# Kernel tuning notes

Measured on AMD Instinct MI355X. Metric: run time of the kernel, lower is better.

The kernel has to match this reference:

```python
import jax, jax.numpy as jnp
import numpy as np

B, T, TR, DIM, H = 1, 4096, 1024, 1536, 12
DH = DIM // H          # 128
EPS = 1e-6             # RMSNorm eps
REF_SCALE = 1.0


def setup_inputs() -> dict:
    key = jax.random.key(0)
    ks = jax.random.split(key, 20)
    s = 0.02
    w = lambda k: jax.random.normal(k, (DIM, DIM), jnp.float32) * s
    b = lambda k: jax.random.normal(k, (DIM,), jnp.float32) * 0.01
    theta = jax.random.uniform(ks[2], (T, DH // 2), jnp.float32) * (2.0 * np.pi)
    return {
        "hidden_states": jax.random.normal(ks[0], (B, T, DIM), jnp.float32),
        "ref_hidden_states": jax.random.normal(ks[1], (B, TR, DIM), jnp.float32),
        "rot_cos": jnp.cos(theta),
        "rot_sin": jnp.sin(theta),
        "Wq": w(ks[3]), "bq": b(ks[4]),
        "Wk": w(ks[5]), "bk": b(ks[6]),
        "Wv": w(ks[7]), "bv": b(ks[8]),
        "Wkr": w(ks[9]), "bkr": b(ks[10]),
        "Wvr": w(ks[11]), "bvr": b(ks[12]),
        "Wo": w(ks[13]), "bo": b(ks[14]),
        "gq": jnp.ones((DIM,), jnp.float32),
        "gk": jnp.ones((DIM,), jnp.float32),
    }


def _rmsnorm(x, g):
    return x * jax.lax.rsqrt(jnp.mean(x * x, axis=-1, keepdims=True) + EPS) * g


def _heads(x):  # [B, T, DIM] -> [B, H, T, DH]
    return x.reshape(B, -1, H, DH).transpose(0, 2, 1, 3)


def _merge(x):  # [B, H, T, DH] -> [B, T, DIM]
    return x.transpose(0, 2, 1, 3).reshape(B, -1, DIM)


def _rope(x, c, s):
    # consecutive pairs along DH form complex numbers (view_as_complex semantics)
    xe, xo = x[..., 0::2], x[..., 1::2]
    c = c[None, None]  # [1,1,T,DH/2]
    s = s[None, None]
    re = xe * c - xo * s
    im = xe * s + xo * c
    return jnp.stack([re, im], axis=-1).reshape(x.shape)


def _attn(q, k, v):
    scale = 1.0 / jnp.sqrt(jnp.asarray(DH, q.dtype))
    p = jax.nn.softmax(jnp.einsum("bhqd,bhkd->bhqk", q, k) * scale, axis=-1)
    return jnp.einsum("bhqk,bhkd->bhqd", p, v)


def reference(hidden_states, ref_hidden_states, rot_cos, rot_sin,
              Wq, bq, Wk, bk, Wv, bv, Wkr, bkr, Wvr, bvr, Wo, bo, gq, gk):
    # QKV projections (self-attention: encoder_hidden_states = hidden_states)
    q_lin = hidden_states @ Wq + bq
    k_lin = hidden_states @ Wk + bk
    v_lin = hidden_states @ Wv + bv

    # ---- reference-attention branch (uses pre-RoPE query) ----
    ref_q = _heads(_rmsnorm(q_lin, gq))
    ref_k = _heads(_rmsnorm(ref_hidden_states @ Wkr + bkr, gk))
    ref_v = _heads(ref_hidden_states @ Wvr + bvr)
    ref_out = _merge(_attn(ref_q, ref_k, ref_v))  # [B, T, DIM]

    # ---- main attention with QK-norm + RoPE ----
    q = _rope(_heads(_rmsnorm(q_lin, gq)), rot_cos, rot_sin)
    k = _rope(_heads(_rmsnorm(k_lin, gk)), rot_cos, rot_sin)
    v = _heads(v_lin)
    main_out = _merge(_attn(q, k, v))  # [B, T, DIM]

    # scaled residual combine + output projection (dropout = identity)
    out = main_out + REF_SCALE * ref_out
    return out @ Wo + bo
```

## Files before the change

kernel.cpp:

```cpp
#include <hip/hip_runtime.h>

typedef unsigned short u16;
typedef unsigned int u32;
typedef __attribute__((ext_vector_type(8))) short short8;
typedef __attribute__((ext_vector_type(4))) float f32x4;

__device__ inline u16 f2b(float f) {
  u32 u = __builtin_bit_cast(u32, f);
  u += 0x7fff + ((u >> 16) & 1);
  return (u16)(u >> 16);
}
__device__ inline float b2f(u16 u) {
  return __builtin_bit_cast(float, (u32)u << 16);
}
__device__ inline u32 pack_bf16_rn(float a, float b) {
  const u32 ua = __builtin_bit_cast(u32, a) + 0x8000u;
  const u32 ub = __builtin_bit_cast(u32, b) + 0x8000u;
  return (ua >> 16) | (ub & 0xffff0000u);
}
__device__ inline void c_store(float* p, float v) { *p = v; }
__device__ inline void c_store(u16* p, float v) { *p = f2b(v); }

__device__ inline float fexp2(float x) {
#if __has_builtin(__builtin_amdgcn_exp2f)
  return __builtin_amdgcn_exp2f(x);
#else
  return exp2f(x);
#endif
}

typedef const __attribute__((address_space(1))) u32 gu32;
typedef __attribute__((address_space(3))) u32 lu32;
__device__ inline void async16(const u16* g, u16* l) {
  __builtin_amdgcn_global_load_lds((gu32*)g, (lu32*)l, 16, 0, 0);
}

#define QS (0.08838834764831843f * 1.4426950408889634f)

template <int MI, typename TC>
__global__ __launch_bounds__(256) void gemm128_kernel(
    const u16* __restrict__ A, long lda,
    const u16* __restrict__ Bt, long ldb,
    TC* __restrict__ C0, TC* __restrict__ C1, TC* __restrict__ C2, long ldc,
    const float* b0, const float* b1, const float* b2,
    int K) {
  __shared__ u16 As[32 * MI * 32];
  __shared__ u16 Bs[128 * 32];

  const int tid = threadIdx.x;
  const int lane = tid & 63;
  const int w = tid >> 6;
  const int r = lane & 15;
  const int quad = lane >> 4;
  const int m0 = blockIdx.y * (32 * MI);
  const int nb = blockIdx.x * 128;
  const int seg = nb / 1536;
  const int nc = nb - seg * 1536;
  TC* C = seg == 0 ? C0 : (seg == 1 ? C1 : C2);
  const float* bias = seg == 0 ? b0 : (seg == 1 ? b1 : b2);

  const int srow = lane >> 2;
  const int sx = ((lane & 3) ^ (srow & 3)) * 8;
  const u16* Ag = A + (size_t)(m0 + w * 8 * MI + srow) * lda + sx;
  const u16* Bg = Bt + (size_t)(nb + w * 32 + srow) * ldb + sx;
  u16* Al[MI / 2];
#pragma unroll
  for (int j = 0; j < MI / 2; ++j) Al[j] = &As[(w * 8 * MI + 16 * j) * 32];
  u16* const Bl0 = &Bs[(w * 32) * 32];
  u16* const Bl1 = &Bs[(w * 32 + 16) * 32];

  const int wm = (w >> 1) * (16 * MI);
  const int wn = (w & 1) * 64;

  f32x4 acc[MI][4];
#pragma unroll
  for (int i = 0; i < MI; ++i)
#pragma unroll
    for (int j = 0; j < 4; ++j) acc[i][j] = (f32x4){0.f, 0.f, 0.f, 0.f};

  const int fco = (quad ^ (r & 3)) * 8;

  for (int kk = 0; kk < K; kk += 32) {
    __syncthreads();
#pragma unroll
    for (int j = 0; j < MI / 2; ++j) async16(Ag + kk + (size_t)(16 * j) * lda, Al[j]);
    async16(Bg + kk, Bl0);
    async16(Bg + kk + 16 * ldb, Bl1);
    __syncthreads();

    short8 af[MI], bf[4];
#pragma unroll
    for (int mi = 0; mi < MI; ++mi)
      af[mi] = *reinterpret_cast<const short8*>(&As[(wm + 16 * mi + r) * 32 + fco]);
#pragma unroll
    for (int ni = 0; ni < 4; ++ni)
      bf[ni] = *reinterpret_cast<const short8*>(&Bs[(wn + 16 * ni + r) * 32 + fco]);
#pragma unroll
    for (int mi = 0; mi < MI; ++mi)
#pragma unroll
      for (int ni = 0; ni < 4; ++ni)
        acc[mi][ni] = __builtin_amdgcn_mfma_f32_16x16x32_bf16(af[mi], bf[ni], acc[mi][ni], 0, 0, 0);
  }

#pragma unroll
  for (int mi = 0; mi < MI; ++mi)
#pragma unroll
    for (int ni = 0; ni < 4; ++ni)
#pragma unroll
      for (int rr = 0; rr < 4; ++rr) {
        const int row = m0 + wm + 16 * mi + 4 * quad + rr;
        const int col = nc + wn + 16 * ni + r;
        c_store(&C[(size_t)row * ldc + col], acc[mi][ni][rr] + bias[col]);
      }
}

__global__ __launch_bounds__(256) void conv2_kernel(
    const float* __restrict__ xa, u16* __restrict__ ya, int n8a,
    const float* __restrict__ xb, u16* __restrict__ yb, int n8b) {
  int i = blockIdx.x * 256 + threadIdx.x;
  const float* x;
  u16* y;
  if (i < n8a) {
    x = xa; y = ya;
  } else {
    i -= n8a;
    if (i >= n8b) return;
    x = xb; y = yb;
  }
  const float4 v0 = reinterpret_cast<const float4*>(x)[2 * i];
  const float4 v1 = reinterpret_cast<const float4*>(x)[2 * i + 1];
  uint4 rv;
  rv.x = (u32)f2b(v0.x) | ((u32)f2b(v0.y) << 16);
  rv.y = (u32)f2b(v0.z) | ((u32)f2b(v0.w) << 16);
  rv.z = (u32)f2b(v1.x) | ((u32)f2b(v1.y) << 16);
  rv.w = (u32)f2b(v1.z) | ((u32)f2b(v1.w) << 16);
  reinterpret_cast<uint4*>(y)[i] = rv;
}

__device__ inline void transconv_body(const float* __restrict__ W, u16* __restrict__ Wt) {
  __shared__ u16 Ls[64 * 72];
  const int tid = threadIdx.x;
  const int k0 = blockIdx.y * 64;
  const int n0 = blockIdx.x * 64;
#pragma unroll
  for (int i = 0; i < 4; ++i) {
    const int c = tid + 256 * i;
    const int row = c >> 4;
    const int c4 = (c & 15) * 4;
    const float4 v = *reinterpret_cast<const float4*>(&W[(size_t)(k0 + row) * 1536 + n0 + c4]);
    Ls[(c4 + 0) * 72 + row] = f2b(v.x);
    Ls[(c4 + 1) * 72 + row] = f2b(v.y);
    Ls[(c4 + 2) * 72 + row] = f2b(v.z);
    Ls[(c4 + 3) * 72 + row] = f2b(v.w);
  }
  __syncthreads();
#pragma unroll
  for (int i = 0; i < 2; ++i) {
    const int c = tid + 256 * i;
    const int n = c >> 3;
    const int kc = (c & 7) * 8;
    u16 tmp[8];
#pragma unroll
    for (int j = 0; j < 8; ++j) tmp[j] = Ls[n * 72 + kc + j];
    *reinterpret_cast<uint4*>(&Wt[(size_t)(n0 + n) * 1536 + k0 + kc]) =
        *reinterpret_cast<const uint4*>(tmp);
  }
}

__global__ __launch_bounds__(256) void transconv6_kernel(
    const float* W0, const float* W1, const float* W2,
    const float* W3, const float* W4, const float* W5,
    u16* T0, u16* T1, u16* T2, u16* T3, u16* T4, u16* T5) {
  const int z = blockIdx.z;
  const float* W = z == 0 ? W0 : z == 1 ? W1 : z == 2 ? W2 : z == 3 ? W3 : z == 4 ? W4 : W5;
  u16* Wt = z == 0 ? T0 : z == 1 ? T1 : z == 2 ? T2 : z == 3 ? T3 : z == 4 ? T4 : T5;
  transconv_body(W, Wt);
}

__global__ __launch_bounds__(256) void rmsnorm3_kernel(
    const u16* xq, const u16* xk, const u16* xkr,
    const float* gq, const float* gk,
    const float* rc, const float* rs,
    u16* oq_plain, u16* oq_rope, u16* ok_rope, u16* okr_plain) {
  __shared__ float red[4];
  const int z = blockIdx.y;
  const int row = blockIdx.x;
  if (z == 2 && row >= 1024) return;
  const u16* x; const float* g; u16* po; u16* pr; float sc;
  if (z == 0)      { x = xq;  g = gq; po = oq_plain; pr = oq_rope; sc = QS;  }
  else if (z == 1) { x = xk;  g = gk; po = nullptr;  pr = ok_rope; sc = 1.f; }
  else             { x = xkr; g = gk; po = okr_plain; pr = nullptr; sc = 1.f; }

  const int tid = threadIdx.x;
  const u32* xr = reinterpret_cast<const u32*>(x + (size_t)row * 1536);
  float xe[3], xo[3];
  float ss = 0.f;
#pragma unroll
  for (int j = 0; j < 3; ++j) {
    const u32 u = xr[tid + 256 * j];
    const float e = b2f((u16)(u & 0xffff));
    const float o = b2f((u16)(u >> 16));
    xe[j] = e; xo[j] = o;
    ss += e * e + o * o;
  }
#pragma unroll
  for (int off = 32; off; off >>= 1) ss += __shfl_xor(ss, off, 64);
  if ((tid & 63) == 0) red[tid >> 6] = ss;
  __syncthreads();
  const float total = red[0] + red[1] + red[2] + red[3];
  const float rinv = rsqrtf(total * (1.0f / 1536.0f) + 1e-6f) * sc;
  u32* po32 = po ? reinterpret_cast<u32*>(po + (size_t)row * 1536) : nullptr;
  u32* pr32 = pr ? reinterpret_cast<u32*>(pr + (size_t)row * 1536) : nullptr;
#pragma unroll
  for (int j = 0; j < 3; ++j) {
    const int p = tid + 256 * j;
    const float2 gg = reinterpret_cast<const float2*>(g)[p];
    const float e = xe[j] * rinv * gg.x;
    const float o = xo[j] * rinv * gg.y;
    if (po32) po32[p] = (u32)f2b(e) | ((u32)f2b(o) << 16);
    if (pr32) {
      const int i = p & 63;
      const float c = rc[row * 64 + i];
      const float s = rs[row * 64 + i];
      const float re = e * c - o * s;
      const float im = e * s + o * c;
      pr32[p] = (u32)f2b(re) | ((u32)f2b(im) << 16);
    }
  }
}

__global__ __launch_bounds__(256) void vtrans2_kernel(
    const u16* __restrict__ V0, u16* __restrict__ Vt0,
    const u16* __restrict__ V1, u16* __restrict__ Vt1) {
  __shared__ u16 Ls[64 * 136];
  const int z = blockIdx.z;
  const int kvLen = z == 0 ? 4096 : 1024;
  const int kv0 = blockIdx.x * 64;
  if (kv0 >= kvLen) return;
  const u16* V = z == 0 ? V0 : V1;
  u16* Vt = z == 0 ? Vt0 : Vt1;
  const int tid = threadIdx.x;
  const int h = blockIdx.y;
#pragma unroll
  for (int i = 0; i < 4; ++i) {
    const int c = tid + 256 * i;
    const int row = c >> 4, c8 = c & 15;
    *reinterpret_cast<uint4*>(&Ls[row * 136 + 8 * c8]) =
        *reinterpret_cast<const uint4*>(V + (size_t)(kv0 + row) * 1536 + h * 128 + 8 * c8);
  }
  __syncthreads();
#pragma unroll
  for (int i = 0; i < 4; ++i) {
    const int c = tid + 256 * i;
    const int d = c >> 3, kc = c & 7;
    u16 tmp[8];
#pragma unroll
    for (int j = 0; j < 8; ++j) tmp[j] = Ls[(8 * kc + j) * 136 + d];
    *reinterpret_cast<uint4*>(Vt + ((size_t)h * 128 + d) * kvLen + kv0 + 8 * kc) =
        *reinterpret_cast<const uint4*>(tmp);
  }
}

__global__ __launch_bounds__(256, 4) void flash_kernel(
    const u16* __restrict__ Q, const u16* __restrict__ K,
    const u16* __restrict__ Vt, float* __restrict__ O,
    u16* __restrict__ Ob, int kvLen, int addO) {
  __shared__ u16 Ks[64 * 128];
  __shared__ u16 Vs[128 * 64];
  __shared__ u16 Pb[4][16 * 40];
  __shared__ float ab[4][16];

  const int tid = threadIdx.x;
  const int lane = tid & 63;
  const int w = tid >> 6;
  const int r = lane & 15;
  const int quad = lane >> 4;
  const int h = blockIdx.y;
  const int q0 = blockIdx.x * 64;
  const int qrow = q0 + 16 * w + r;
  const int sw = r & 7;

  short8 qf[4];
  {
    const u16* qbase = Q + (size_t)qrow * 1536 + h * 128 + 8 * quad;
#pragma unroll
    for (int ks = 0; ks < 4; ++ks)
      qf[ks] = *reinterpret_cast<const short8*>(qbase + 32 * ks);
  }

  const u16* Kb = K + h * 128;
  const u16* Vb = Vt + (size_t)h * 128 * kvLen;
  u32 koff[4], voff[4];
  int klo[4], vlo[4];
  {
    const int p16 = lane & 15, rin = lane >> 4;
    const int p8 = lane & 7, din = lane >> 3;
#pragma unroll
    for (int j = 0; j < 4; ++j) {
      const int row = 16 * w + 4 * j + rin;
      koff[j] = (u32)row * 1536u + 8u * (u32)(p16 ^ (row & 15));
      klo[j] = (16 * w + 4 * j) * 128;
      const int d = 32 * w + 8 * j + din;
      voff[j] = (u32)d * (u32)kvLen + 8u * (u32)(p8 ^ (d & 7));
      vlo[j] = (32 * w + 8 * j) * 64;
    }
  }

  f32x4 Oc[8];
#pragma unroll
  for (int dt = 0; dt < 8; ++dt) Oc[dt] = (f32x4){0.f, 0.f, 0.f, 0.f};
  float m_i = -1e30f, l_i = 0.f;

  const int nt = kvLen >> 6;
  for (int t = 0; t < nt; ++t) {
    __syncthreads();
    {
      const size_t ko = (size_t)t * (64 * 1536);
      const size_t vo = (size_t)t * 64;
#pragma unroll
      for (int j = 0; j < 4; ++j) async16(Kb + ko + koff[j], &Ks[klo[j]]);
#pragma unroll
      for (int j = 0; j < 4; ++j) async16(Vb + vo + voff[j], &Vs[vlo[j]]);
    }
    __syncthreads();

    f32x4 St[4];
#pragma unroll
    for (int mt = 0; mt < 4; ++mt) St[mt] = (f32x4){0.f, 0.f, 0.f, 0.f};
#pragma unroll
    for (int mt = 0; mt < 4; ++mt) {
      const u16* kp = &Ks[(16 * mt + r) * 128];
#pragma unroll
      for (int ks = 0; ks < 4; ++ks) {
        const short8 af = *reinterpret_cast<const short8*>(kp + 8 * ((quad + 4 * ks) ^ r));
        St[mt] = __builtin_amdgcn_mfma_f32_16x16x32_bf16(af, qf[ks], St[mt], 0, 0, 0);
      }
    }

    float mloc = -1e30f;
#pragma unroll
    for (int mt = 0; mt < 4; ++mt)
#pragma unroll
      for (int rr = 0; rr < 4; ++rr) mloc = fmaxf(mloc, St[mt][rr]);
    mloc = fmaxf(mloc, __shfl_xor(mloc, 16, 64));
    mloc = fmaxf(mloc, __shfl_xor(mloc, 32, 64));
    const float mn = fmaxf(m_i, mloc);

    float alpha = 1.0f;
    if (__any(mloc > m_i)) {
      alpha = fexp2(m_i - mn);
      if (quad == 0) ab[w][r] = alpha;
      const float4 a4 = *reinterpret_cast<const float4*>(&ab[w][4 * quad]);
#pragma unroll
      for (int dt = 0; dt < 8; ++dt) {
        Oc[dt][0] *= a4.x; Oc[dt][1] *= a4.y; Oc[dt][2] *= a4.z; Oc[dt][3] *= a4.w;
      }
    }

    float psum = 0.f;
    uint2 pk[4];
#pragma unroll
    for (int mt = 0; mt < 4; ++mt) {
      const float p0 = fexp2(St[mt][0] - mn);
      const float p1 = fexp2(St[mt][1] - mn);
      const float p2 = fexp2(St[mt][2] - mn);
      const float p3 = fexp2(St[mt][3] - mn);
      psum += (p0 + p1) + (p2 + p3);
      pk[mt].x = pack_bf16_rn(p0, p1);
      pk[mt].y = pack_bf16_rn(p2, p3);
    }
    psum += __shfl_xor(psum, 16, 64);
    psum += __shfl_xor(psum, 32, 64);
    l_i = l_i * alpha + psum;
    m_i = mn;

#pragma unroll
    for (int mt = 0; mt < 2; ++mt)
      *reinterpret_cast<uint2*>(&Pb[w][r * 40 + 16 * mt + 4 * quad]) = pk[mt];
    {
      const short8 pa0 = *reinterpret_cast<const short8*>(&Pb[w][r * 40 + 8 * quad]);
#pragma unroll
      for (int dt = 0; dt < 8; ++dt) {
        const int d = 16 * dt + r;
        const short8 b0 = *reinterpret_cast<const short8*>(&Vs[d * 64 + 8 * (quad ^ sw)]);
        Oc[dt] = __builtin_amdgcn_mfma_f32_16x16x32_bf16(pa0, b0, Oc[dt], 0, 0, 0);
      }
    }
#pragma unroll
    for (int mt = 2; mt < 4; ++mt)
      *reinterpret_cast<uint2*>(&Pb[w][r * 40 + 16 * (mt - 2) + 4 * quad]) = pk[mt];
    {
      const short8 pa1 = *reinterpret_cast<const short8*>(&Pb[w][r * 40 + 8 * quad]);
#pragma unroll
      for (int dt = 0; dt < 8; ++dt) {
        const int d = 16 * dt + r;
        const short8 b1 = *reinterpret_cast<const short8*>(&Vs[d * 64 + 8 * ((4 + quad) ^ sw)]);
        Oc[dt] = __builtin_amdgcn_mfma_f32_16x16x32_bf16(pa1, b1, Oc[dt], 0, 0, 0);
      }
    }
  }

  if (quad == 0) ab[w][r] = 1.0f / l_i;
  const float4 li4 = *reinterpret_cast<const float4*>(&ab[w][4 * quad]);
  const float lv[4] = {li4.x, li4.y, li4.z, li4.w};
  float* obf = O + (size_t)(q0 + 16 * w) * 1536 + h * 128;
  u16* obb = Ob + (size_t)(q0 + 16 * w) * 1536 + h * 128;
#pragma unroll
  for (int rr = 0; rr < 4; ++rr) {
    float* orow = obf + (size_t)(4 * quad + rr) * 1536 + r;
    u16* brow = obb + (size_t)(4 * quad + rr) * 1536 + r;
#pragma unroll
    for (int dt = 0; dt < 8; ++dt) {
      float v = Oc[dt][rr] * lv[rr];
      if (addO) {
        v += orow[16 * dt];
        brow[16 * dt] = f2b(v);
      } else {
        orow[16 * dt] = v;
      }
    }
  }
}

extern "C" void kernel_launch(void* const* d_in, const int* in_sizes, int n_in,
                              void* d_out, int out_size, void* d_ws, size_t ws_size,
                              hipStream_t stream) {
  (void)in_sizes; (void)n_in; (void)out_size; (void)ws_size;
  constexpr int T = 4096, TR = 1024, DIM = 1536, NH = 12;

  const float* hs  = (const float*)d_in[0];
  const float* rhs = (const float*)d_in[1];
  const float* rc  = (const float*)d_in[2];
  const float* rs  = (const float*)d_in[3];
  const float* Wq  = (const float*)d_in[4];
  const float* bq  = (const float*)d_in[5];
  const float* Wk  = (const float*)d_in[6];
  const float* bk  = (const float*)d_in[7];
  const float* Wv  = (const float*)d_in[8];
  const float* bv  = (const float*)d_in[9];
  const float* Wkr = (const float*)d_in[10];
  const float* bkr = (const float*)d_in[11];
  const float* Wvr = (const float*)d_in[12];
  const float* bvr = (const float*)d_in[13];
  const float* Wo  = (const float*)d_in[14];
  const float* bo  = (const float*)d_in[15];
  const float* gq  = (const float*)d_in[16];
  const float* gk  = (const float*)d_in[17];
  float* out = (float*)d_out;

  char* ws = (char*)d_ws;
  size_t off = 0;
  auto alloc = [&](size_t bytes) -> void* {
    void* p = ws + off;
    off += (bytes + 255) & ~(size_t)255;
    return p;
  };
  u16* bQ    = (u16*)alloc((size_t)T * DIM * 2);
  u16* bQr   = (u16*)alloc((size_t)T * DIM * 2);
  u16* bK    = (u16*)alloc((size_t)T * DIM * 2);
  u16* bV    = (u16*)alloc((size_t)T * DIM * 2);
  u16* bKr   = (u16*)alloc((size_t)TR * DIM * 2);
  u16* bVr   = (u16*)alloc((size_t)TR * DIM * 2);
  float* bO  = (float*)alloc((size_t)T * DIM * 4);
  u16* bHs   = (u16*)alloc((size_t)T * DIM * 2);
  u16* bRhs  = (u16*)alloc((size_t)TR * DIM * 2);
  u16* bWqkv = (u16*)alloc((size_t)3 * DIM * DIM * 2);
  u16* bWr   = (u16*)alloc((size_t)2 * DIM * DIM * 2);
  u16* bWoT  = (u16*)alloc((size_t)DIM * DIM * 2);
  u16* VtG = bHs;
  u16* VtR = bRhs;
  u16* bOb = bWqkv;

  const dim3 blk(256);

  conv2_kernel<<<dim3((T * DIM / 8 + TR * DIM / 8 + 255) / 256), blk, 0, stream>>>(
      hs, bHs, T * DIM / 8, rhs, bRhs, TR * DIM / 8);

  transconv6_kernel<<<dim3(24, 24, 6), blk, 0, stream>>>(
      Wq, Wk, Wv, Wkr, Wvr, Wo,
      bWqkv + 0 * (size_t)DIM * DIM, bWqkv + 1 * (size_t)DIM * DIM,
      bWqkv + 2 * (size_t)DIM * DIM, bWr + 0 * (size_t)DIM * DIM,
      bWr + 1 * (size_t)DIM * DIM, bWoT);

  gemm128_kernel<4, u16><<<dim3(36, 32), blk, 0, stream>>>(
      bHs, DIM, bWqkv, DIM, bQ, bK, bV, DIM, bq, bk, bv, DIM);
  gemm128_kernel<2, u16><<<dim3(24, 16), blk, 0, stream>>>(
      bRhs, DIM, bWr, DIM, bKr, bVr, (u16*)nullptr, DIM, bkr, bvr, nullptr, DIM);

  rmsnorm3_kernel<<<dim3(T, 3), blk, 0, stream>>>(
      bQ, bK, bKr, gq, gk, rc, rs, bQ, bQr, bK, bKr);

  vtrans2_kernel<<<dim3(T / 64, NH, 2), blk, 0, stream>>>(bV, VtG, bVr, VtR);

  flash_kernel<<<dim3(T / 64, NH), blk, 0, stream>>>(bQ, bKr, VtR, bO, bOb, TR, 0);
  flash_kernel<<<dim3(T / 64, NH), blk, 0, stream>>>(bQr, bK, VtG, bO, bOb, T, 1);

  gemm128_kernel<2, float><<<dim3(12, 64), blk, 0, stream>>>(
      bOb, DIM, bWoT, DIM, out, (float*)nullptr, (float*)nullptr, DIM, bo, nullptr, nullptr, DIM);
}
```

Baseline: 537.7 us.

## Double-buffer K/V tiles in flash kernel with lazy softmax rescaling

The flash attention loop now uses 32-row K/V tiles in two LDS buffers. The next tile is prefetched asynchronously while the current one is computed, which removes one barrier per iteration and overlaps global loads with MFMA work. Online-softmax rescaling is skipped unless the running max grows by more than a threshold, and MFMA sections are wrapped in s_setprio. The trade-offs are half-size tiles, which mean more iterations and barriers, and unnormalized exponentials that can grow to a bounded but larger range before the bf16 packing.

```diff
diff --git a/kernel.cpp b/kernel.cpp
--- a/kernel.cpp
+++ b/kernel.cpp
@@ -265,8 +265,8 @@
     const u16* __restrict__ Q, const u16* __restrict__ K,
     const u16* __restrict__ Vt, float* __restrict__ O,
     u16* __restrict__ Ob, int kvLen, int addO) {
-  __shared__ u16 Ks[64 * 128];
-  __shared__ u16 Vs[128 * 64];
+  __shared__ u16 Ks[2][32 * 128];
+  __shared__ u16 Vs[2][128 * 32];
   __shared__ u16 Pb[4][16 * 40];
   __shared__ float ab[4][16];
 
@@ -278,7 +278,7 @@
   const int h = blockIdx.y;
   const int q0 = blockIdx.x * 64;
   const int qrow = q0 + 16 * w + r;
-  const int sw = r & 7;
+  const int s3 = r & 3;
 
   short8 qf[4];
   {
@@ -290,19 +290,19 @@
 
   const u16* Kb = K + h * 128;
   const u16* Vb = Vt + (size_t)h * 128 * kvLen;
-  u32 koff[4], voff[4];
-  int klo[4], vlo[4];
+  u32 koff[2], voff[2];
+  int klo[2], vlo[2];
   {
     const int p16 = lane & 15, rin = lane >> 4;
-    const int p8 = lane & 7, din = lane >> 3;
-#pragma unroll
-    for (int j = 0; j < 4; ++j) {
-      const int row = 16 * w + 4 * j + rin;
+    const int p4 = lane & 3, din = lane >> 2;
+#pragma unroll
+    for (int j = 0; j < 2; ++j) {
+      const int row = 8 * w + 4 * j + rin;
       koff[j] = (u32)row * 1536u + 8u * (u32)(p16 ^ (row & 15));
-      klo[j] = (16 * w + 4 * j) * 128;
-      const int d = 32 * w + 8 * j + din;
-      voff[j] = (u32)d * (u32)kvLen + 8u * (u32)(p8 ^ (d & 7));
-      vlo[j] = (32 * w + 8 * j) * 64;
+      klo[j] = (8 * w + 4 * j) * 128;
+      const int d = 32 * w + 16 * j + din;
+      voff[j] = (u32)d * (u32)kvLen + 8u * (u32)(p4 ^ (d & 3));
+      vlo[j] = (32 * w + 16 * j) * 32;
     }
   }
 
@@ -311,44 +311,56 @@
   for (int dt = 0; dt < 8; ++dt) Oc[dt] = (f32x4){0.f, 0.f, 0.f, 0.f};
   float m_i = -1e30f, l_i = 0.f;
 
-  const int nt = kvLen >> 6;
+  const int nt = kvLen >> 5;
+
+  {
+    const size_t ko0 = 0, vo0 = 0;
+#pragma unroll
+    for (int j = 0; j < 2; ++j) async16(Kb + ko0 + koff[j], &Ks[0][klo[j]]);
+#pragma unroll
+    for (int j = 0; j < 2; ++j) async16(Vb + vo0 + voff[j], &Vs[0][vlo[j]]);
+  }
+
   for (int t = 0; t < nt; ++t) {
+    const int buf = t & 1;
     __syncthreads();
-    {
-      const size_t ko = (size_t)t * (64 * 1536);
-      const size_t vo = (size_t)t * 64;
-#pragma unroll
-      for (int j = 0; j < 4; ++j) async16(Kb + ko + koff[j], &Ks[klo[j]]);
-#pragma unroll
-      for (int j = 0; j < 4; ++j) async16(Vb + vo + voff[j], &Vs[vlo[j]]);
-    }
-    __syncthreads();
-
-    f32x4 St[4];
-#pragma unroll
-    for (int mt = 0; mt < 4; ++mt) St[mt] = (f32x4){0.f, 0.f, 0.f, 0.f};
-#pragma unroll
-    for (int mt = 0; mt < 4; ++mt) {
-      const u16* kp = &Ks[(16 * mt + r) * 128];
+    if (t + 1 < nt) {
+      const size_t ko = (size_t)(t + 1) * (32 * 1536);
+      const size_t vo = (size_t)(t + 1) * 32;
+#pragma unroll
+      for (int j = 0; j < 2; ++j) async16(Kb + ko + koff[j], &Ks[buf ^ 1][klo[j]]);
+#pragma unroll
+      for (int j = 0; j < 2; ++j) async16(Vb + vo + voff[j], &Vs[buf ^ 1][vlo[j]]);
+    }
+
+    f32x4 St[2];
+#pragma unroll
+    for (int mt = 0; mt < 2; ++mt) St[mt] = (f32x4){0.f, 0.f, 0.f, 0.f};
+    __builtin_amdgcn_s_setprio(1);
+#pragma unroll
+    for (int mt = 0; mt < 2; ++mt) {
+      const u16* kp = &Ks[buf][(16 * mt + r) * 128];
 #pragma unroll
       for (int ks = 0; ks < 4; ++ks) {
         const short8 af = *reinterpret_cast<const short8*>(kp + 8 * ((quad + 4 * ks) ^ r));
         St[mt] = __builtin_amdgcn_mfma_f32_16x16x32_bf16(af, qf[ks], St[mt], 0, 0, 0);
       }
     }
+    __builtin_amdgcn_s_setprio(0);
 
     float mloc = -1e30f;
 #pragma unroll
-    for (int mt = 0; mt < 4; ++mt)
+    for (int mt = 0; mt < 2; ++mt)
 #pragma unroll
       for (int rr = 0; rr < 4; ++rr) mloc = fmaxf(mloc, St[mt][rr]);
     mloc = fmaxf(mloc, __shfl_xor(mloc, 16, 64));
     mloc = fmaxf(mloc, __shfl_xor(mloc, 32, 64));
-    const float mn = fmaxf(m_i, mloc);
 
     float alpha = 1.0f;
-    if (__any(mloc > m_i)) {
+    if (__any(mloc > m_i + 11.5f)) {
+      const float mn = fmaxf(m_i, mloc);
       alpha = fexp2(m_i - mn);
+      m_i = mn;
       if (quad == 0) ab[w][r] = alpha;
       const float4 a4 = *reinterpret_cast<const float4*>(&ab[w][4 * quad]);
 #pragma unroll
@@ -358,13 +370,13 @@
     }
 
     float psum = 0.f;
-    uint2 pk[4];
-#pragma unroll
-    for (int mt = 0; mt < 4; ++mt) {
-      const float p0 = fexp2(St[mt][0] - mn);
-      const float p1 = fexp2(St[mt][1] - mn);
-      const float p2 = fexp2(St[mt][2] - mn);
-      const float p3 = fexp2(St[mt][3] - mn);
+    uint2 pk[2];
+#pragma unroll
+    for (int mt = 0; mt < 2; ++mt) {
+      const float p0 = fexp2(St[mt][0] - m_i);
+      const float p1 = fexp2(St[mt][1] - m_i);
+      const float p2 = fexp2(St[mt][2] - m_i);
+      const float p3 = fexp2(St[mt][3] - m_i);
       psum += (p0 + p1) + (p2 + p3);
       pk[mt].x = pack_bf16_rn(p0, p1);
       pk[mt].y = pack_bf16_rn(p2, p3);
@@ -372,31 +384,20 @@
     psum += __shfl_xor(psum, 16, 64);
     psum += __shfl_xor(psum, 32, 64);
     l_i = l_i * alpha + psum;
-    m_i = mn;
 
 #pragma unroll
     for (int mt = 0; mt < 2; ++mt)
       *reinterpret_cast<uint2*>(&Pb[w][r * 40 + 16 * mt + 4 * quad]) = pk[mt];
     {
-      const short8 pa0 = *reinterpret_cast<const short8*>(&Pb[w][r * 40 + 8 * quad]);
+      const short8 pa = *reinterpret_cast<const short8*>(&Pb[w][r * 40 + 8 * quad]);
+      __builtin_amdgcn_s_setprio(1);
 #pragma unroll
       for (int dt = 0; dt < 8; ++dt) {
         const int d = 16 * dt + r;
-        const short8 b0 = *reinterpret_cast<const short8*>(&Vs[d * 64 + 8 * (quad ^ sw)]);
-        Oc[dt] = __builtin_amdgcn_mfma_f32_16x16x32_bf16(pa0, b0, Oc[dt], 0, 0, 0);
+        const short8 b0 = *reinterpret_cast<const short8*>(&Vs[buf][d * 32 + 8 * (quad ^ s3)]);
+        Oc[dt] = __builtin_amdgcn_mfma_f32_16x16x32_bf16(pa, b0, Oc[dt], 0, 0, 0);
       }
-    }
-#pragma unroll
-    for (int mt = 2; mt < 4; ++mt)
-      *reinterpret_cast<uint2*>(&Pb[w][r * 40 + 16 * (mt - 2) + 4 * quad]) = pk[mt];
-    {
-      const short8 pa1 = *reinterpret_cast<const short8*>(&Pb[w][r * 40 + 8 * quad]);
-#pragma unroll
-      for (int dt = 0; dt < 8; ++dt) {
-        const int d = 16 * dt + r;
-        const short8 b1 = *reinterpret_cast<const short8*>(&Vs[d * 64 + 8 * ((4 + quad) ^ sw)]);
-        Oc[dt] = __builtin_amdgcn_mfma_f32_16x16x32_bf16(pa1, b1, Oc[dt], 0, 0, 0);
-      }
+      __builtin_amdgcn_s_setprio(0);
     }
   }
 
```

Result: slower. 564.1 us (+4.9%).
